# Optimization experiments

Hardware: AMD Instinct MI355X
Metric: run time of the kernel (lower is better)

The kernel has to match this reference:

```python
import jax, jax.numpy as jnp
import numpy as np

EPS = 1e-6
NH, HD, D, FF = 4, 128, 512, 2048
SCALE = HD ** -0.5


def rms(x, w):
    return x * jax.lax.rsqrt(jnp.mean(x * x, axis=-1, keepdims=True) + EPS) * w


def adaln(x, emb, w, b, nw):
    e = jax.nn.silu(emb) @ w.T + b  # [B, 6D]
    sm, cm, gm, sp, cp, gp = jnp.split(e, 6, axis=-1)
    y = rms(x, nw) * (1.0 + cm[:, None]) + sm[:, None]
    return y, gm, sp, cp, gp


def apply_rope(x, rope):
    # x: [B,H,N,HD], rope: [N,1,HD] (even slots cos-source, odd slots sin-source)
    f = rope[:, 0]  # [N, HD]
    cos = jnp.repeat(f[:, 0::2], 2, axis=-1)[None, None]  # [1,1,N,HD]
    sin = jnp.repeat(f[:, 1::2], 2, axis=-1)[None, None]
    xr = x.reshape(*x.shape[:-1], -1, 2)
    rot = jnp.stack([-xr[..., 1], xr[..., 0]], axis=-1).reshape(x.shape)
    return x * cos + rot * sin


def sdpa(q, k, v, scale):
    s = jnp.einsum('bhqd,bhkd->bhqk', q, k) * scale
    p = jax.nn.softmax(s, axis=-1)
    return jnp.einsum('bhqk,bhkd->bhqd', p, v)


def mlp(x, w1, b1, w2, b2):
    h = jax.nn.gelu(x @ w1.T + b1, approximate=True)
    return h @ w2.T + b2


def setup_inputs() -> dict:
    key = jax.random.key(0)
    ks = jax.random.split(key, 32)
    B, L, Hh, Ww = 2, 512, 64, 32
    N = Hh * Ww
    s = 1.0 / np.sqrt(D)
    sf = 1.0 / np.sqrt(FF)
    rn = lambda k, sh, sc=1.0: jax.random.normal(k, sh, jnp.float32) * sc
    # RoPE buffer: per-pair angles, even slots cos, odd slots sin
    pos = jnp.arange(N, dtype=jnp.float32)
    inv = 1.0 / (10000.0 ** (jnp.arange(0, HD, 2, dtype=jnp.float32) / HD))
    ang = pos[:, None] * inv[None, :]  # [N, HD//2]
    rope = jnp.zeros((N, 1, HD), jnp.float32)
    rope = rope.at[:, 0, 0::2].set(jnp.cos(ang)).at[:, 0, 1::2].set(jnp.sin(ang))
    return {
        'txt': rn(ks[0], (B, L, D)),
        'img': rn(ks[1], (B, N, D)),
        'vec': rn(ks[2], (B, D)),
        'rope': rope,
        'sol_temperature': jax.random.uniform(ks[3], (B, NH), jnp.float32) + 0.5,
        'sol_spatial': rn(ks[4], (B, 8, 8)),
        'img_adaln_w': rn(ks[5], (6 * D, D), s), 'img_adaln_b': rn(ks[6], (6 * D,), 0.02),
        'img_adaln_norm_w': jnp.ones((D,), jnp.float32),
        'txt_adaln_w': rn(ks[7], (6 * D, D), s), 'txt_adaln_b': rn(ks[8], (6 * D,), 0.02),
        'txt_adaln_norm_w': jnp.ones((D,), jnp.float32),
        'txt_qkv_w': rn(ks[9], (3 * NH * HD, D), s),
        'img_qkv_w': rn(ks[10], (3 * NH * HD, D), s),
        'txt_out_w': rn(ks[11], (D, NH * HD), s),
        'img_out_w': rn(ks[12], (D, NH * HD), s),
        'sol_mod_w': rn(ks[13], (NH,), 0.1), 'sol_mod_b': rn(ks[14], (NH,), 0.1),
        'img_norm2_w': jnp.ones((D,), jnp.float32),
        'txt_norm2_w': jnp.ones((D,), jnp.float32),
        'img_fc1_w': rn(ks[15], (FF, D), s), 'img_fc1_b': rn(ks[16], (FF,), 0.02),
        'img_fc2_w': rn(ks[17], (D, FF), sf), 'img_fc2_b': rn(ks[18], (D,), 0.02),
        'txt_fc1_w': rn(ks[19], (FF, D), s), 'txt_fc1_b': rn(ks[20], (FF,), 0.02),
        'txt_fc2_w': rn(ks[21], (D, FF), sf), 'txt_fc2_b': rn(ks[22], (D,), 0.02),
        'H': Hh, 'W': Ww,
    }


def reference(txt, img, vec, rope, sol_temperature, sol_spatial,
              img_adaln_w, img_adaln_b, img_adaln_norm_w,
              txt_adaln_w, txt_adaln_b, txt_adaln_norm_w,
              txt_qkv_w, img_qkv_w, txt_out_w, img_out_w,
              sol_mod_w, sol_mod_b, img_norm2_w, txt_norm2_w,
              img_fc1_w, img_fc1_b, img_fc2_w, img_fc2_b,
              txt_fc1_w, txt_fc1_b, txt_fc2_w, txt_fc2_b, H, W):
    B, L, _ = txt.shape
    N = img.shape[1]
    img_n, img_g, img_sh, img_sc, img_gm = adaln(img, vec, img_adaln_w, img_adaln_b, img_adaln_norm_w)
    txt_n, txt_g, txt_sh, txt_sc, txt_gm = adaln(txt, vec, txt_adaln_w, txt_adaln_b, txt_adaln_norm_w)
    # joint attention
    tqkv = (txt_n @ txt_qkv_w.T).reshape(B, L, 3, NH, HD)
    iqkv = (img_n @ img_qkv_w.T).reshape(B, N, 3, NH, HD)
    tq, tk, tv = [jnp.transpose(tqkv[:, :, i], (0, 2, 1, 3)) for i in range(3)]
    iq, ik, iv = [jnp.transpose(iqkv[:, :, i], (0, 2, 1, 3)) for i in range(3)]
    iq = apply_rope(iq, rope)
    ik = apply_rope(ik, rope)
    # spatial prior modulation (1x1 conv over bilinear-upsampled prior)
    sol_up = jax.image.resize(sol_spatial[:, None], (B, 1, H, W), method='bilinear')
    mod = sol_up * sol_mod_w[None, :, None, None] + sol_mod_b[None, :, None, None]  # [B,NH,H,W]
    mod = jnp.exp(jnp.clip(mod.reshape(B, NH, H * W), -2.0, 2.0))
    iq = iq * mod[..., None]
    ik = ik * mod[..., None]
    k = jnp.concatenate([tk, ik], axis=2)  # [B,NH,L+N,HD]
    v = jnp.concatenate([tv, iv], axis=2)
    txt_att = sdpa(tq, k, v, SCALE)
    txt_att = jnp.transpose(txt_att, (0, 2, 1, 3)).reshape(B, L, NH * HD) @ txt_out_w.T
    # temperature-rescaled image attention
    temp = jnp.maximum(jnp.mean(sol_temperature, axis=1, keepdims=True), 0.1)  # [B,1]
    eff = (SCALE / temp)[:, :, None, None]  # [B,1,1,1]
    img_att = sdpa(iq * jnp.sqrt(eff), k * jnp.sqrt(eff), v, 1.0)
    img_att = jnp.transpose(img_att, (0, 2, 1, 3)).reshape(B, N, NH * HD) @ img_out_w.T
    txt = txt + txt_g[:, None] * txt_att
    img = img + img_g[:, None] * img_att
    txt_in = rms(txt, txt_norm2_w) * (1.0 + txt_sc[:, None]) + txt_sh[:, None]
    img_in = rms(img, img_norm2_w) * (1.0 + img_sc[:, None]) + img_sh[:, None]
    txt = txt + txt_gm[:, None] * mlp(txt_in, txt_fc1_w, txt_fc1_b, txt_fc2_w, txt_fc2_b)
    img = img + img_gm[:, None] * mlp(img_in, img_fc1_w, img_fc1_b, img_fc2_w, img_fc2_b)
    return (txt, img)
```

## Files before the change

### kernel.cpp

```cpp
#include <hip/hip_runtime.h>
#include <math.h>

typedef unsigned short ushort_t;

constexpr int B_  = 2;
constexpr int L_  = 512;
constexpr int N_  = 2048;
constexpr int T_  = 2560;
constexpr int D_  = 512;
constexpr int NH_ = 4;
constexpr int HD_ = 128;
constexpr int FF_ = 2048;
constexpr int SIXD = 3072;
constexpr int MROWS = B_ * T_;
#define SCALE_ 0.08838834764831843f

constexpr size_t QSZ    = (size_t)B_ * NH_ * T_ * HD_;
constexpr size_t O_ETXT = 0;
constexpr size_t O_EIMG = O_ETXT + (size_t)B_ * SIXD;
constexpr size_t O_MOD  = O_EIMG + (size_t)B_ * SIXD;
constexpr size_t O_EFF  = O_MOD + (size_t)B_ * NH_ * N_;
constexpr size_t O_XN   = O_EFF + 16;
constexpr size_t O_Q    = O_XN + QSZ;
constexpr size_t O_K    = O_Q + QSZ;
constexpr size_t O_V    = O_K + QSZ;
constexpr size_t O_ATTN = O_V + QSZ;
constexpr size_t O_X2   = O_ATTN + QSZ;
constexpr size_t O_XIN2 = O_X2 + QSZ;
constexpr size_t O_H    = O_Q;

constexpr size_t WQ_STREAM = (size_t)SIXD / 2 * D_;
constexpr size_t WQ_TOTAL  = 2 * WQ_STREAM;
constexpr size_t WM_PROJ   = 0;
constexpr size_t WM_PROJ_S = (size_t)D_ * D_;
constexpr size_t WM_FC1    = WM_PROJ + 2 * WM_PROJ_S;
constexpr size_t WM_FC1_S  = (size_t)FF_ * D_;
constexpr size_t WM_FC2    = WM_FC1 + 2 * WM_FC1_S;
constexpr size_t WM_FC2_S  = (size_t)D_ * FF_;

typedef short bf16x8 __attribute__((ext_vector_type(8)));
typedef float f32x4 __attribute__((ext_vector_type(4)));

__device__ __forceinline__ ushort_t f2bf_rne(float x) {
  unsigned u = __float_as_uint(x);
  u += 0x7fff + ((u >> 16) & 1);
  return (ushort_t)(u >> 16);
}

__global__ __launch_bounds__(256) void k_stage0(
    const float* __restrict__ vec,
    const float* __restrict__ wt, const float* __restrict__ bt,
    const float* __restrict__ wi, const float* __restrict__ bi,
    const float* __restrict__ sspat, const float* __restrict__ mw,
    const float* __restrict__ mb, const float* __restrict__ stemp,
    const float* __restrict__ qkvwt, const float* __restrict__ qkvwi,
    float* __restrict__ ws) {
  int blk = blockIdx.x;
  if (blk < 48) {
    int s = blk / 24;
    int rem = blk % 24;
    int b = rem / 12;
    int o = (rem % 12) * 256 + threadIdx.x;
    __shared__ float sv[D_];
    for (int i = threadIdx.x; i < D_; i += 256) {
      float x = vec[b * D_ + i];
      sv[i] = x / (1.0f + __expf(-x));
    }
    __syncthreads();
    const float* w = (s == 0) ? wt : wi;
    const float* bb = (s == 0) ? bt : bi;
    const float4* wrow = (const float4*)(w + (size_t)o * D_);
    float acc = 0.f;
    for (int d4 = 0; d4 < D_ / 4; ++d4) {
      float4 wv = wrow[d4];
      int d = d4 * 4;
      acc += wv.x * sv[d] + wv.y * sv[d + 1] + wv.z * sv[d + 2] + wv.w * sv[d + 3];
    }
    acc += bb[o];
    float* e = ws + ((s == 0) ? O_ETXT : O_EIMG);
    e[b * SIXD + o] = acc;
  } else if (blk < 112) {
    int idx = (blk - 48) * 256 + threadIdx.x;
    if (idx < B_) {
      float s = 0.f;
      for (int h = 0; h < NH_; ++h) s += stemp[idx * NH_ + h];
      float t = fmaxf(s * 0.25f, 0.1f);
      ws[O_EFF + idx] = SCALE_ / t;
    }
    int b = idx / (NH_ * N_);
    int h = (idx / N_) % NH_;
    int n = idx % N_;
    int y = n >> 5;
    int x = n & 31;
    float fy = (y + 0.5f) * 0.125f - 0.5f;
    float fx = (x + 0.5f) * 0.25f  - 0.5f;
    float y0f = floorf(fy), x0f = floorf(fx);
    float wy = fy - y0f, wx = fx - x0f;
    int y0 = (int)y0f, x0 = (int)x0f;
    int iy0 = y0 < 0 ? 0 : y0, iy1 = (y0 + 1) > 7 ? 7 : (y0 + 1);
    int ix0 = x0 < 0 ? 0 : x0, ix1 = (x0 + 1) > 7 ? 7 : (x0 + 1);
    const float* S = sspat + b * 64;
    float v00 = S[iy0*8+ix0], v01 = S[iy0*8+ix1];
    float v10 = S[iy1*8+ix0], v11 = S[iy1*8+ix1];
    float up = (1.f-wy)*((1.f-wx)*v00 + wx*v01) + wy*((1.f-wx)*v10 + wx*v11);
    float m = up * mw[h] + mb[h];
    m = fminf(fmaxf(m, -2.f), 2.f);
    ws[O_MOD + idx] = __expf(m);
  } else {
    int g = (blk - 112) * 256 + threadIdx.x;
    int s = g >= (int)(WQ_STREAM / 4);
    const float4* src = (const float4*)(s ? qkvwi : qkvwt);
    float4 v = src[g - s * (int)(WQ_STREAM / 4)];
    ushort4 hh, ll;
    hh.x = f2bf_rne(v.x); hh.y = f2bf_rne(v.y); hh.z = f2bf_rne(v.z); hh.w = f2bf_rne(v.w);
    ll.x = f2bf_rne(v.x - __uint_as_float((unsigned)hh.x << 16));
    ll.y = f2bf_rne(v.y - __uint_as_float((unsigned)hh.y << 16));
    ll.z = f2bf_rne(v.z - __uint_as_float((unsigned)hh.z << 16));
    ll.w = f2bf_rne(v.w - __uint_as_float((unsigned)hh.w << 16));
    ushort_t* Wqh = (ushort_t*)(ws + O_ATTN);
    ushort_t* Wql = Wqh + WQ_TOTAL;
    *(ushort4*)&Wqh[(size_t)g * 4] = hh;
    *(ushort4*)&Wql[(size_t)g * 4] = ll;
  }
}

template<bool FROM_INPUT>
__global__ __launch_bounds__(256) void k_rmsmod(const float* __restrict__ txt, const float* __restrict__ img,
                                                const float* __restrict__ src_ws,
                                                const float* __restrict__ nw_txt, const float* __restrict__ nw_img,
                                                int sh_off, int sc_off,
                                                const float* __restrict__ e_ws,
                                                ushort_t* __restrict__ oh, ushort_t* __restrict__ ol) {
  int row = blockIdx.x;
  int b = row / T_;
  int t = row % T_;
  bool is_txt = t < L_;
  int i0 = threadIdx.x * 2;
  float x0, x1;
  if (FROM_INPUT) {
    const float* src = is_txt ? (txt + ((size_t)b * L_ + t) * D_)
                              : (img + ((size_t)b * N_ + (t - L_)) * D_);
    x0 = src[i0]; x1 = src[i0 + 1];
  } else {
    const float* src = src_ws + (size_t)row * D_;
    x0 = src[i0]; x1 = src[i0 + 1];
  }
  float ss = x0 * x0 + x1 * x1;
  for (int off = 32; off; off >>= 1) ss += __shfl_down(ss, off, 64);
  __shared__ float red[4];
  if ((threadIdx.x & 63) == 0) red[threadIdx.x >> 6] = ss;
  __syncthreads();
  float tot = red[0] + red[1] + red[2] + red[3];
  float r = rsqrtf(tot * (1.0f / D_) + 1e-6f);
  const float* e = e_ws + (is_txt ? O_ETXT : O_EIMG) + (size_t)b * SIXD;
  const float* nw = is_txt ? nw_txt : nw_img;
  float y0 = x0 * r * nw[i0]     * (1.f + e[sc_off + i0])     + e[sh_off + i0];
  float y1 = x1 * r * nw[i0 + 1] * (1.f + e[sc_off + i0 + 1]) + e[sh_off + i0 + 1];
  ushort_t h0 = f2bf_rne(y0), h1 = f2bf_rne(y1);
  ushort_t l0 = f2bf_rne(y0 - __uint_as_float((unsigned)h0 << 16));
  ushort_t l1 = f2bf_rne(y1 - __uint_as_float((unsigned)h1 << 16));
  *(unsigned*)&oh[(size_t)row * D_ + i0] = (unsigned)h0 | ((unsigned)h1 << 16);
  *(unsigned*)&ol[(size_t)row * D_ + i0] = (unsigned)l0 | ((unsigned)l1 << 16);
}

template<int NTILE, int NTERMS, int KDIM, int NPR, int EPI>
__global__ __launch_bounds__(256) void k_gemm(
    const ushort_t* __restrict__ Aph, const ushort_t* __restrict__ Apl,
    const ushort_t* __restrict__ Wth, const ushort_t* __restrict__ Wtl,
    const ushort_t* __restrict__ Wih, const ushort_t* __restrict__ Wil,
    const float* __restrict__ biast, const float* __restrict__ biasi,
    const float* __restrict__ ws_ro, float* __restrict__ wsw,
    const float* __restrict__ txt, const float* __restrict__ img,
    ushort_t* __restrict__ Hph, ushort_t* __restrict__ Hpl, float* __restrict__ outf) {
  int mt = blockIdx.x / NPR, nt = blockIdx.x % NPR;
  int row0 = mt * 128;
  int col0 = nt * NTILE;
  int b = row0 / T_;
  int t0 = row0 % T_;
  bool is_txt = t0 < L_;
  const ushort_t* Wh = is_txt ? Wth : Wih;
  const ushort_t* Wl = (NTERMS == 3) ? (is_txt ? Wtl : Wil) : nullptr;

  __shared__ __align__(16) ushort_t ash[128 * 40];
  __shared__ __align__(16) ushort_t asl[128 * 40];
  __shared__ __align__(16) ushort_t bsh[NTILE * 40];
  __shared__ __align__(16) ushort_t bsl[(NTERMS == 3) ? NTILE * 40 : 8];

  int tid = threadIdx.x;
  int w = tid >> 6, lane = tid & 63, quad = lane >> 4, lc = lane & 15;
  int rh = w >> 1, ch = w & 1;
  constexpr int NFR = NTILE / 32;

  f32x4 acc[4][NFR];
  #pragma unroll
  for (int m = 0; m < 4; ++m)
    #pragma unroll
    for (int n = 0; n < NFR; ++n) acc[m][n] = f32x4{0.f, 0.f, 0.f, 0.f};

  for (int kt = 0; kt < KDIM / 32; ++kt) {
    {
      int r = tid >> 1, koff = (tid & 1) * 16;
      size_t abase = (size_t)(row0 + r) * KDIM + kt * 32 + koff;
      uint4 h0 = *(const uint4*)&Aph[abase];
      uint4 h1 = *(const uint4*)&Aph[abase + 8];
      uint4 l0 = *(const uint4*)&Apl[abase];
      uint4 l1 = *(const uint4*)&Apl[abase + 8];
      *(uint4*)&ash[r * 40 + koff]     = h0;
      *(uint4*)&ash[r * 40 + koff + 8] = h1;
      *(uint4*)&asl[r * 40 + koff]     = l0;
      *(uint4*)&asl[r * 40 + koff + 8] = l1;
    }
    {
      constexpr int NU = NTILE / 64;
      #pragma unroll
      for (int u = 0; u < NU; ++u) {
        int idx = u * 256 + tid;
        int rw = idx >> 2, c8 = (idx & 3) * 8;
        size_t wb = (size_t)(col0 + rw) * KDIM + kt * 32 + c8;
        *(uint4*)&bsh[rw * 40 + c8] = *(const uint4*)&Wh[wb];
        if (NTERMS == 3) *(uint4*)&bsl[rw * 40 + c8] = *(const uint4*)&Wl[wb];
      }
    }
    __syncthreads();

    bf16x8 afh[4], afl[4];
    #pragma unroll
    for (int m = 0; m < 4; ++m) {
      int ar = rh * 64 + m * 16 + lc;
      afh[m] = *(const bf16x8*)&ash[ar * 40 + quad * 8];
      afl[m] = *(const bf16x8*)&asl[ar * 40 + quad * 8];
    }
    #pragma unroll
    for (int n = 0; n < NFR; ++n) {
      int br = ch * (NTILE / 2) + n * 16 + lc;
      bf16x8 bh = *(const bf16x8*)&bsh[br * 40 + quad * 8];
      if (NTERMS == 3) {
        bf16x8 bl = *(const bf16x8*)&bsl[br * 40 + quad * 8];
        #pragma unroll
        for (int m = 0; m < 4; ++m) {
          acc[m][n] = __builtin_amdgcn_mfma_f32_16x16x32_bf16(afl[m], bh, acc[m][n], 0, 0, 0);
          acc[m][n] = __builtin_amdgcn_mfma_f32_16x16x32_bf16(afh[m], bl, acc[m][n], 0, 0, 0);
          acc[m][n] = __builtin_amdgcn_mfma_f32_16x16x32_bf16(afh[m], bh, acc[m][n], 0, 0, 0);
        }
      } else {
        #pragma unroll
        for (int m = 0; m < 4; ++m) {
          acc[m][n] = __builtin_amdgcn_mfma_f32_16x16x32_bf16(afl[m], bh, acc[m][n], 0, 0, 0);
          acc[m][n] = __builtin_amdgcn_mfma_f32_16x16x32_bf16(afh[m], bh, acc[m][n], 0, 0, 0);
        }
      }
    }
    __syncthreads();
  }

  const float* e = ws_ro + (is_txt ? O_ETXT : O_EIMG) + (size_t)b * SIXD;
  const float* bias = is_txt ? biast : biasi;
  #pragma unroll
  for (int m = 0; m < 4; ++m) {
    #pragma unroll
    for (int n = 0; n < NFR; ++n) {
      #pragma unroll
      for (int r = 0; r < 4; ++r) {
        int rg = row0 + rh * 64 + m * 16 + quad * 4 + r;
        int cg = col0 + ch * (NTILE / 2) + n * 16 + lc;
        float val = acc[m][n][r];
        int tt = rg % T_;
        if (EPI == 0) {
          int which = cg >> 9, h = (cg >> 7) & 3, dd = cg & 127;
          float* dst = wsw + (which == 0 ? O_Q : which == 1 ? O_K : O_V)
                     + (((size_t)b * NH_ + h) * T_ + tt) * HD_ + dd;
          *dst = val;
        } else if (EPI == 1) {
          float g = e[1024 + cg];
          float res = is_txt ? txt[((size_t)b * L_ + tt) * D_ + cg]
                             : img[((size_t)b * N_ + (tt - L_)) * D_ + cg];
          wsw[O_X2 + (size_t)rg * D_ + cg] = res + g * val;
        } else if (EPI == 2) {
          float x = val + bias[cg];
          float z = 0.7978845608028654f * (x + 0.044715f * x * x * x);
          z = fminf(fmaxf(z, -40.f), 40.f);
          float u = __expf(-2.f * z);
          float th = (1.f - u) / (1.f + u);
          float hv = 0.5f * x * (1.f + th);
          ushort_t hh = f2bf_rne(hv);
          Hph[(size_t)rg * FF_ + cg] = hh;
          Hpl[(size_t)rg * FF_ + cg] = f2bf_rne(hv - __uint_as_float((unsigned)hh << 16));
        } else {
          float g = e[2560 + cg];
          float v2 = ws_ro[O_X2 + (size_t)rg * D_ + cg] + g * (val + bias[cg]);
          size_t oi = is_txt ? ((size_t)b * L_ + tt) * D_ + cg
                             : (size_t)B_ * L_ * D_ + ((size_t)b * N_ + (tt - L_)) * D_ + cg;
          outf[oi] = v2;
        }
      }
    }
  }
}

__global__ __launch_bounds__(256) void k_stage1(
    float* __restrict__ ws, const float* __restrict__ rope,
    const float* __restrict__ pw_t, const float* __restrict__ pw_i,
    const float* __restrict__ f1_t, const float* __restrict__ f1_i,
    const float* __restrict__ f2_t, const float* __restrict__ f2_i) {
  int blk = blockIdx.x;
  if (blk < 5120) {
    int idx = blk * 256 + threadIdx.x;
    int i = idx & 63;
    int p = idx >> 6;
    int t = p % T_;
    int bh = p / T_;
    size_t base = (size_t)p * HD_ + 2 * i;
    float* Q = ws + O_Q;
    float* K = ws + O_K;
    float k0 = K[base], k1 = K[base + 1];
    if (t >= L_) {
      int n = t - L_;
      float c = rope[(size_t)n * HD_ + 2 * i];
      float s = rope[(size_t)n * HD_ + 2 * i + 1];
      float m = ws[O_MOD + (size_t)bh * N_ + n];
      float q0 = Q[base], q1 = Q[base + 1];
      Q[base]     = (q0 * c - q1 * s) * m;
      Q[base + 1] = (q1 * c + q0 * s) * m;
      float nk0 = (k0 * c - k1 * s) * m;
      float nk1 = (k1 * c + k0 * s) * m;
      k0 = nk0; k1 = nk1;
    }
    ushort_t h0 = f2bf_rne(k0), h1 = f2bf_rne(k1);
    ushort_t l0 = f2bf_rne(k0 - __uint_as_float((unsigned)h0 << 16));
    ushort_t l1 = f2bf_rne(k1 - __uint_as_float((unsigned)h1 << 16));
    ushort_t* KH = (ushort_t*)(ws + O_XIN2);
    ushort_t* KL = KH + QSZ;
    *(unsigned*)&KH[(size_t)p * HD_ + 2 * i] = (unsigned)h0 | ((unsigned)h1 << 16);
    *(unsigned*)&KL[(size_t)p * HD_ + 2 * i] = (unsigned)l0 | ((unsigned)l1 << 16);
  } else if (blk < 5440) {
    int vblk = blk - 5120;
    int bh = vblk & 7;
    int tt = vblk >> 3;
    int t0 = tt * 64;
    __shared__ ushort_t vls[128 * 72];
    int tid = threadIdx.x;
    {
      int tr = tid & 63, dc = tid >> 6;
      const float4* src = (const float4*)(ws + O_V + ((size_t)bh * T_ + t0 + tr) * HD_ + dc * 32);
      #pragma unroll
      for (int f = 0; f < 8; ++f) {
        float4 v = src[f];
        int d = dc * 32 + f * 4;
        vls[(d + 0) * 72 + tr] = f2bf_rne(v.x);
        vls[(d + 1) * 72 + tr] = f2bf_rne(v.y);
        vls[(d + 2) * 72 + tr] = f2bf_rne(v.z);
        vls[(d + 3) * 72 + tr] = f2bf_rne(v.w);
      }
    }
    __syncthreads();
    {
      int d = tid >> 1, th = (tid & 1) * 32;
      unsigned* Vt32 = (unsigned*)(ws + O_X2);
      size_t obase = (((size_t)bh * HD_ + d) * T_ + t0 + th) >> 1;
      #pragma unroll
      for (int k = 0; k < 16; ++k) {
        unsigned lo = vls[d * 72 + th + 2 * k];
        unsigned hi = vls[d * 72 + th + 2 * k + 1];
        Vt32[obase + k] = lo | (hi << 16);
      }
    }
  } else {
    int g = (blk - 5440) * 256 + threadIdx.x;
    const float* src; int local;
    if (g < 65536)        { src = pw_t; local = g; }
    else if (g < 131072)  { src = pw_i; local = g - 65536; }
    else if (g < 393216)  { src = f1_t; local = g - 131072; }
    else if (g < 655360)  { src = f1_i; local = g - 393216; }
    else if (g < 917504)  { src = f2_t; local = g - 655360; }
    else                  { src = f2_i; local = g - 917504; }
    float4 v = ((const float4*)src)[local];
    ushort4 hh;
    hh.x = f2bf_rne(v.x); hh.y = f2bf_rne(v.y); hh.z = f2bf_rne(v.z); hh.w = f2bf_rne(v.w);
    ushort_t* Wm = (ushort_t*)(ws + O_XN);
    *(ushort4*)&Wm[(size_t)g * 4] = hh;
  }
}

__global__ __launch_bounds__(256) void k_attn6(const float* __restrict__ ws_ro, float* __restrict__ wsw) {
  int bh = blockIdx.x & 7;
  int qg = blockIdx.x >> 3;
  int b = bh >> 2, h = bh & 3;
  int tid = threadIdx.x;
  int w = tid >> 6, lane = tid & 63, quad = lane >> 4, lc = lane & 15;
  int q0 = (qg * 4 + w) * 16;
  float scale = (q0 < L_) ? SCALE_ : ws_ro[O_EFF + b];

  const ushort_t* Khs = (const ushort_t*)(ws_ro + O_XIN2);
  const ushort_t* Kls = Khs + QSZ;
  const ushort_t* Vts = (const ushort_t*)(ws_ro + O_X2) + (size_t)bh * HD_ * T_;

  __shared__ __align__(16) ushort_t ksh[64 * 136];
  __shared__ __align__(16) ushort_t ksl[64 * 136];
  __shared__ __align__(16) ushort_t ps[4 * 16 * 72];
  ushort_t* pw = &ps[w * 1152];

  bf16x8 qh[4], ql[4];
  {
    const float* qrowp = ws_ro + O_Q + ((size_t)bh * T_ + q0 + lc) * HD_ + quad * 8;
    #pragma unroll
    for (int k2 = 0; k2 < 4; ++k2) {
      float4 a = *(const float4*)(qrowp + k2 * 32);
      float4 c = *(const float4*)(qrowp + k2 * 32 + 4);
      float v[8] = {a.x, a.y, a.z, a.w, c.x, c.y, c.z, c.w};
      #pragma unroll
      for (int e = 0; e < 8; ++e) {
        float x = v[e] * scale;
        ushort_t hh = f2bf_rne(x);
        float hf = __uint_as_float((unsigned)hh << 16);
        qh[k2][e] = (short)hh;
        ql[k2][e] = (short)f2bf_rne(x - hf);
      }
    }
  }

  f32x4 o[8];
  #pragma unroll
  for (int i = 0; i < 8; ++i) o[i] = f32x4{0.f, 0.f, 0.f, 0.f};
  float m_r[4] = {-1e30f, -1e30f, -1e30f, -1e30f};
  float l_r[4] = {0.f, 0.f, 0.f, 0.f};

  for (int kt = 0; kt < T_ / 64; ++kt) {
    {
      int row = tid >> 2, cs = tid & 3;
      size_t gbase = ((size_t)bh * T_ + kt * 64 + row) * HD_;
      #pragma unroll
      for (int cc = 0; cc < 4; ++cc) {
        int c = cs + cc * 4;
        *(uint4*)&ksh[row * 136 + c * 8] = *(const uint4*)&Khs[gbase + c * 8];
        *(uint4*)&ksl[row * 136 + c * 8] = *(const uint4*)&Kls[gbase + c * 8];
      }
    }
    __syncthreads();

    f32x4 s[4];
    #pragma unroll
    for (int nt = 0; nt < 4; ++nt) s[nt] = f32x4{0.f, 0.f, 0.f, 0.f};
    #pragma unroll
    for (int k2 = 0; k2 < 4; ++k2) {
      int ko = k2 * 32 + quad * 8;
      #pragma unroll
      for (int nt = 0; nt < 4; ++nt) {
        bf16x8 kh = *(const bf16x8*)&ksh[(nt * 16 + lc) * 136 + ko];
        bf16x8 kl = *(const bf16x8*)&ksl[(nt * 16 + lc) * 136 + ko];
        s[nt] = __builtin_amdgcn_mfma_f32_16x16x32_bf16(ql[k2], kh, s[nt], 0, 0, 0);
        s[nt] = __builtin_amdgcn_mfma_f32_16x16x32_bf16(qh[k2], kl, s[nt], 0, 0, 0);
        s[nt] = __builtin_amdgcn_mfma_f32_16x16x32_bf16(qh[k2], kh, s[nt], 0, 0, 0);
      }
    }

    const ushort_t* Vb = Vts + kt * 64;
    bf16x8 vb0[8];
    #pragma unroll
    for (int dt = 0; dt < 8; ++dt)
      vb0[dt] = *(const bf16x8*)&Vb[(size_t)(dt * 16 + lc) * T_ + quad * 8];

    float alpha[4];
    #pragma unroll
    for (int r = 0; r < 4; ++r) {
      float rm = fmaxf(fmaxf(s[0][r], s[1][r]), fmaxf(s[2][r], s[3][r]));
      rm = fmaxf(rm, __shfl_xor(rm, 1, 64));
      rm = fmaxf(rm, __shfl_xor(rm, 2, 64));
      rm = fmaxf(rm, __shfl_xor(rm, 4, 64));
      rm = fmaxf(rm, __shfl_xor(rm, 8, 64));
      float mn = fmaxf(m_r[r], rm);
      alpha[r] = __expf(m_r[r] - mn);
      m_r[r] = mn;
      float p0 = __expf(s[0][r] - mn);
      float p1 = __expf(s[1][r] - mn);
      float p2 = __expf(s[2][r] - mn);
      float p3 = __expf(s[3][r] - mn);
      float rs = (p0 + p1) + (p2 + p3);
      rs += __shfl_xor(rs, 1, 64);
      rs += __shfl_xor(rs, 2, 64);
      rs += __shfl_xor(rs, 4, 64);
      rs += __shfl_xor(rs, 8, 64);
      l_r[r] = l_r[r] * alpha[r] + rs;
      int prow = quad * 4 + r;
      pw[prow * 72 + lc]      = f2bf_rne(p0);
      pw[prow * 72 + lc + 16] = f2bf_rne(p1);
      pw[prow * 72 + lc + 32] = f2bf_rne(p2);
      pw[prow * 72 + lc + 48] = f2bf_rne(p3);
    }
    #pragma unroll
    for (int dt = 0; dt < 8; ++dt) {
      #pragma unroll
      for (int r = 0; r < 4; ++r) o[dt][r] *= alpha[r];
    }

    bf16x8 vb1[8];
    #pragma unroll
    for (int dt = 0; dt < 8; ++dt)
      vb1[dt] = *(const bf16x8*)&Vb[(size_t)(dt * 16 + lc) * T_ + 32 + quad * 8];

    bf16x8 pa0 = *(const bf16x8*)&pw[lc * 72 + quad * 8];
    bf16x8 pa1 = *(const bf16x8*)&pw[lc * 72 + 32 + quad * 8];
    #pragma unroll
    for (int dt = 0; dt < 8; ++dt)
      o[dt] = __builtin_amdgcn_mfma_f32_16x16x32_bf16(pa0, vb0[dt], o[dt], 0, 0, 0);
    #pragma unroll
    for (int dt = 0; dt < 8; ++dt)
      o[dt] = __builtin_amdgcn_mfma_f32_16x16x32_bf16(pa1, vb1[dt], o[dt], 0, 0, 0);
    __syncthreads();
  }

  ushort_t* ATh = (ushort_t*)(wsw + O_ATTN);
  ushort_t* ATl = ATh + QSZ;
  int trow0 = q0 + quad * 4;
  #pragma unroll
  for (int r = 0; r < 4; ++r) {
    float inv = 1.0f / l_r[r];
    size_t base = ((size_t)b * T_ + (trow0 + r)) * D_ + h * HD_ + lc;
    #pragma unroll
    for (int dt = 0; dt < 8; ++dt) {
      float v = o[dt][r] * inv;
      ushort_t hh = f2bf_rne(v);
      ATh[base + dt * 16] = hh;
      ATl[base + dt * 16] = f2bf_rne(v - __uint_as_float((unsigned)hh << 16));
    }
  }
}

extern "C" void kernel_launch(void* const* d_in, const int* in_sizes, int n_in,
                              void* d_out, int out_size, void* d_ws, size_t ws_size,
                              hipStream_t stream) {
  (void)in_sizes; (void)n_in; (void)out_size; (void)ws_size;
  const float* txt    = (const float*)d_in[0];
  const float* img    = (const float*)d_in[1];
  const float* vec    = (const float*)d_in[2];
  const float* rope   = (const float*)d_in[3];
  const float* stemp  = (const float*)d_in[4];
  const float* sspat  = (const float*)d_in[5];
  const float* i_aw   = (const float*)d_in[6];
  const float* i_ab   = (const float*)d_in[7];
  const float* i_anw  = (const float*)d_in[8];
  const float* t_aw   = (const float*)d_in[9];
  const float* t_ab   = (const float*)d_in[10];
  const float* t_anw  = (const float*)d_in[11];
  const float* t_qkvw = (const float*)d_in[12];
  const float* i_qkvw = (const float*)d_in[13];
  const float* t_outw = (const float*)d_in[14];
  const float* i_outw = (const float*)d_in[15];
  const float* modw   = (const float*)d_in[16];
  const float* modb   = (const float*)d_in[17];
  const float* i_n2w  = (const float*)d_in[18];
  const float* t_n2w  = (const float*)d_in[19];
  const float* i_f1w  = (const float*)d_in[20];
  const float* i_f1b  = (const float*)d_in[21];
  const float* i_f2w  = (const float*)d_in[22];
  const float* i_f2b  = (const float*)d_in[23];
  const float* t_f1w  = (const float*)d_in[24];
  const float* t_f1b  = (const float*)d_in[25];
  const float* t_f2w  = (const float*)d_in[26];
  const float* t_f2b  = (const float*)d_in[27];
  float* ws = (float*)d_ws;
  float* out = (float*)d_out;
  ushort_t* XNh  = (ushort_t*)(ws + O_XN);   ushort_t* XNl  = XNh + QSZ;
  ushort_t* ATh  = (ushort_t*)(ws + O_ATTN); ushort_t* ATl  = ATh + QSZ;
  ushort_t* XI2h = (ushort_t*)(ws + O_XIN2); ushort_t* XI2l = XI2h + QSZ;
  ushort_t* Hh   = (ushort_t*)(ws + O_H);    ushort_t* Hl   = Hh + 4 * QSZ;
  ushort_t* Wqh = (ushort_t*)(ws + O_ATTN);  ushort_t* Wql = Wqh + WQ_TOTAL;
  ushort_t* Wm  = (ushort_t*)(ws + O_XN);

  hipLaunchKernelGGL(k_stage0, dim3(48 + 64 + 1536), dim3(256), 0, stream,
                     vec, t_aw, t_ab, i_aw, i_ab, sspat, modw, modb, stemp,
                     t_qkvw, i_qkvw, ws);
  hipLaunchKernelGGL((k_rmsmod<true>), dim3(MROWS), dim3(256), 0, stream,
                     txt, img, (const float*)nullptr, t_anw, i_anw, 0, 512, ws, XNh, XNl);
  hipLaunchKernelGGL((k_gemm<128, 3, 512, 12, 0>), dim3(40 * 12), dim3(256), 0, stream,
                     XNh, XNl, Wqh, Wql, Wqh + WQ_STREAM, Wql + WQ_STREAM,
                     nullptr, nullptr, ws, ws, txt, img,
                     (ushort_t*)nullptr, (ushort_t*)nullptr, nullptr);
  hipLaunchKernelGGL(k_stage1, dim3(5120 + 320 + 4608), dim3(256), 0, stream,
                     ws, rope, t_outw, i_outw, t_f1w, i_f1w, t_f2w, i_f2w);
  hipLaunchKernelGGL(k_attn6, dim3(320), dim3(256), 0, stream, ws, ws);
  hipLaunchKernelGGL((k_gemm<64, 2, 512, 8, 1>), dim3(40 * 8), dim3(256), 0, stream,
                     ATh, ATl, Wm + WM_PROJ, nullptr, Wm + WM_PROJ + WM_PROJ_S, nullptr,
                     nullptr, nullptr, ws, ws, txt, img,
                     (ushort_t*)nullptr, (ushort_t*)nullptr, nullptr);
  hipLaunchKernelGGL((k_rmsmod<false>), dim3(MROWS), dim3(256), 0, stream,
                     (const float*)nullptr, (const float*)nullptr, ws + O_X2, t_n2w, i_n2w,
                     1536, 2048, ws, XI2h, XI2l);
  hipLaunchKernelGGL((k_gemm<128, 2, 512, 16, 2>), dim3(40 * 16), dim3(256), 0, stream,
                     XI2h, XI2l, Wm + WM_FC1, nullptr, Wm + WM_FC1 + WM_FC1_S, nullptr,
                     t_f1b, i_f1b, ws, ws, txt, img, Hh, Hl, nullptr);
  hipLaunchKernelGGL((k_gemm<64, 2, 2048, 8, 3>), dim3(40 * 8), dim3(256), 0, stream,
                     Hh, Hl, Wm + WM_FC2, nullptr, Wm + WM_FC2 + WM_FC2_S, nullptr,
                     t_f2b, i_f2b, ws, ws, txt, img,
                     (ushort_t*)nullptr, (ushort_t*)nullptr, out);
}
```

Before: 564.8 us.

## Split attention over three key chunks and merge partials in a combine kernel

The attention kernel now splits the key loop into three ranges, so it launches three times as many blocks. Each block writes unnormalised fp32 partial outputs plus per-row max and sum into scratch regions that are free at that point. A new combine kernel rescales the three partials with log-sum-exp weights, normalises them, and writes the split bf16 hi/lo attention output into the old Q area. This targets poor CU occupancy from the previous 320-block grid, at the cost of extra global traffic for the fp32 partials and one more launch.

Result: faster. 513.6 us (-9.1%).

```diff
diff --git a/kernel.cpp b/kernel.cpp
--- a/kernel.cpp
+++ b/kernel.cpp
@@ -28,6 +28,7 @@
 constexpr size_t O_X2   = O_ATTN + QSZ;
 constexpr size_t O_XIN2 = O_X2 + QSZ;
 constexpr size_t O_H    = O_Q;
+constexpr size_t O_ML   = O_X2 + QSZ / 2;
 
 constexpr size_t WQ_STREAM = (size_t)SIXD / 2 * D_;
 constexpr size_t WQ_TOTAL  = 2 * WQ_STREAM;
@@ -381,10 +382,14 @@
   }
 }
 
-__global__ __launch_bounds__(256) void k_attn6(const float* __restrict__ ws_ro, float* __restrict__ wsw) {
+__global__ __launch_bounds__(256) void k_attn7(const float* __restrict__ ws_ro, float* __restrict__ wsw) {
   int bh = blockIdx.x & 7;
-  int qg = blockIdx.x >> 3;
-  int b = bh >> 2, h = bh & 3;
+  int rest = blockIdx.x >> 3;
+  int qg = rest % 40;
+  int ks = rest / 40;
+  int kt0 = (ks == 0) ? 0 : (ks == 1) ? 14 : 27;
+  int kt1 = (ks == 0) ? 14 : (ks == 1) ? 27 : 40;
+  int b = bh >> 2;
   int tid = threadIdx.x;
   int w = tid >> 6, lane = tid & 63, quad = lane >> 4, lc = lane & 15;
   int q0 = (qg * 4 + w) * 16;
@@ -424,7 +429,7 @@
   float m_r[4] = {-1e30f, -1e30f, -1e30f, -1e30f};
   float l_r[4] = {0.f, 0.f, 0.f, 0.f};
 
-  for (int kt = 0; kt < T_ / 64; ++kt) {
+  for (int kt = kt0; kt < kt1; ++kt) {
     {
       int row = tid >> 2, cs = tid & 3;
       size_t gbase = ((size_t)bh * T_ + kt * 64 + row) * HD_;
@@ -508,20 +513,73 @@
     __syncthreads();
   }
 
-  ushort_t* ATh = (ushort_t*)(wsw + O_ATTN);
-  ushort_t* ATl = ATh + QSZ;
+  float* OP = wsw + ((ks == 0) ? O_K : (ks == 1) ? O_V : O_ATTN);
+  float* ML = wsw + O_ML;
   int trow0 = q0 + quad * 4;
   #pragma unroll
   for (int r = 0; r < 4; ++r) {
-    float inv = 1.0f / l_r[r];
-    size_t base = ((size_t)b * T_ + (trow0 + r)) * D_ + h * HD_ + lc;
-    #pragma unroll
-    for (int dt = 0; dt < 8; ++dt) {
-      float v = o[dt][r] * inv;
-      ushort_t hh = f2bf_rne(v);
-      ATh[base + dt * 16] = hh;
-      ATl[base + dt * 16] = f2bf_rne(v - __uint_as_float((unsigned)hh << 16));
-    }
+    size_t base = ((size_t)bh * T_ + (trow0 + r)) * HD_ + lc;
+    #pragma unroll
+    for (int dt = 0; dt < 8; ++dt) OP[base + dt * 16] = o[dt][r];
+    if (lc == 0) {
+      size_t mi = (((size_t)ks * 8 + bh) * T_ + (trow0 + r)) * 2;
+      ML[mi]     = m_r[r];
+      ML[mi + 1] = l_r[r];
+    }
+  }
+}
+
+__global__ __launch_bounds__(256) void k_comb(const float* __restrict__ ws_ro, float* __restrict__ wsw) {
+  int bh = blockIdx.x & 7;
+  int qg = blockIdx.x >> 3;
+  int b = bh >> 2, h = bh & 3;
+  int q0 = qg * 64;
+  int tid = threadIdx.x;
+  __shared__ float wls[64][4];
+  if (tid < 64) {
+    const float* ML = ws_ro + O_ML;
+    size_t r0 = ((size_t)0 * 8 + bh) * T_ + q0 + tid;
+    size_t r1 = ((size_t)1 * 8 + bh) * T_ + q0 + tid;
+    size_t r2 = ((size_t)2 * 8 + bh) * T_ + q0 + tid;
+    float m0 = ML[r0 * 2], l0 = ML[r0 * 2 + 1];
+    float m1 = ML[r1 * 2], l1 = ML[r1 * 2 + 1];
+    float m2 = ML[r2 * 2], l2 = ML[r2 * 2 + 1];
+    float mm = fmaxf(fmaxf(m0, m1), m2);
+    float w0 = __expf(m0 - mm), w1 = __expf(m1 - mm), w2 = __expf(m2 - mm);
+    float inv = 1.0f / (w0 * l0 + w1 * l1 + w2 * l2);
+    wls[tid][0] = w0 * inv; wls[tid][1] = w1 * inv; wls[tid][2] = w2 * inv; wls[tid][3] = 0.f;
+  }
+  __syncthreads();
+  const float* P0 = ws_ro + O_K;
+  const float* P1 = ws_ro + O_V;
+  const float* P2 = ws_ro + O_ATTN;
+  ushort_t* ATh = (ushort_t*)(wsw + O_Q);
+  ushort_t* ATl = ATh + QSZ;
+  #pragma unroll
+  for (int it = 0; it < 8; ++it) {
+    int idx = it * 256 + tid;
+    int row = idx >> 5;
+    int d4 = (idx & 31) * 4;
+    size_t pb = ((size_t)bh * T_ + q0 + row) * HD_ + d4;
+    float4 a = *(const float4*)&P0[pb];
+    float4 c = *(const float4*)&P1[pb];
+    float4 d = *(const float4*)&P2[pb];
+    float w0 = wls[row][0], w1 = wls[row][1], w2 = wls[row][2];
+    float v[4] = {a.x * w0 + c.x * w1 + d.x * w2,
+                  a.y * w0 + c.y * w1 + d.y * w2,
+                  a.z * w0 + c.z * w1 + d.z * w2,
+                  a.w * w0 + c.w * w1 + d.w * w2};
+    ushort4 hh, ll;
+    ushort_t* hp = (ushort_t*)&hh; ushort_t* lp = (ushort_t*)&ll;
+    #pragma unroll
+    for (int j = 0; j < 4; ++j) {
+      ushort_t hv = f2bf_rne(v[j]);
+      hp[j] = hv;
+      lp[j] = f2bf_rne(v[j] - __uint_as_float((unsigned)hv << 16));
+    }
+    size_t ob = ((size_t)b * T_ + q0 + row) * D_ + h * HD_ + d4;
+    *(ushort4*)&ATh[ob] = hh;
+    *(ushort4*)&ATl[ob] = ll;
   }
 }
 
@@ -560,9 +618,9 @@
   float* ws = (float*)d_ws;
   float* out = (float*)d_out;
   ushort_t* XNh  = (ushort_t*)(ws + O_XN);   ushort_t* XNl  = XNh + QSZ;
-  ushort_t* ATh  = (ushort_t*)(ws + O_ATTN); ushort_t* ATl  = ATh + QSZ;
   ushort_t* XI2h = (ushort_t*)(ws + O_XIN2); ushort_t* XI2l = XI2h + QSZ;
   ushort_t* Hh   = (ushort_t*)(ws + O_H);    ushort_t* Hl   = Hh + 4 * QSZ;
+  ushort_t* ATh  = (ushort_t*)(ws + O_Q);    ushort_t* ATl  = ATh + QSZ;
   ushort_t* Wqh = (ushort_t*)(ws + O_ATTN);  ushort_t* Wql = Wqh + WQ_TOTAL;
   ushort_t* Wm  = (ushort_t*)(ws + O_XN);
 
@@ -577,7 +635,8 @@
                      (ushort_t*)nullptr, (ushort_t*)nullptr, nullptr);
   hipLaunchKernelGGL(k_stage1, dim3(5120 + 320 + 4608), dim3(256), 0, stream,
                      ws, rope, t_outw, i_outw, t_f1w, i_f1w, t_f2w, i_f2w);
-  hipLaunchKernelGGL(k_attn6, dim3(320), dim3(256), 0, stream, ws, ws);
+  hipLaunchKernelGGL(k_attn7, dim3(960), dim3(256), 0, stream, ws, ws);
+  hipLaunchKernelGGL(k_comb, dim3(320), dim3(256), 0, stream, ws, ws);
   hipLaunchKernelGGL((k_gemm<64, 2, 512, 8, 1>), dim3(40 * 8), dim3(256), 0, stream,
                      ATh, ATl, Wm + WM_PROJ, nullptr, Wm + WM_PROJ + WM_PROJ_S, nullptr,
                      nullptr, nullptr, ws, ws, txt, img,
```
